# Kernel tuning notes

Hardware: AMD Instinct MI355X
Metric: run time of the kernel (lower is better)

The kernel has to match this reference:

```python
import jax, jax.numpy as jnp
import numpy as np

EPS = 1e-5
N_ENT, N_REL, DIM = 100000, 500, 128
B, K = 2048, 128

def _norm(x):
    # stable L2 norm over last dim, keepdims
    return jnp.sqrt(jnp.sum(x * x, axis=-1, keepdims=True) + 1e-15)

def norm_within_one(x):
    # project onto the open unit ball (Poincare ball, c=1)
    n = _norm(x)
    maxn = 1.0 - EPS
    return jnp.where(n > maxn, x * (maxn / n), x)

def p_log_map(x):
    # log map at the origin: artanh(||x||) * x / ||x||
    n = jnp.clip(_norm(x), EPS, 1.0 - EPS)
    return jnp.arctanh(n) * x / n

def p_exp_map(v):
    # exp map at the origin: tanh(||v||) * v / ||v||
    n = jnp.clip(_norm(v), EPS, None)
    return jnp.tanh(n) * v / n

def p_sum(x, y):
    # Mobius addition (c=1)
    xy = jnp.sum(x * y, axis=-1, keepdims=True)
    x2 = jnp.sum(x * x, axis=-1, keepdims=True)
    y2 = jnp.sum(y * y, axis=-1, keepdims=True)
    num = (1.0 + 2.0 * xy + y2) * x + (1.0 - x2) * y
    den = 1.0 + 2.0 * xy + x2 * y2
    return num / jnp.clip(den, EPS, None)

def calculate_dist(x, y):
    # Poincare distance: arccosh(1 + 2||x-y||^2 / ((1-||x||^2)(1-||y||^2)))
    x2 = jnp.sum(x * x, axis=-1)
    y2 = jnp.sum(y * y, axis=-1)
    d2 = jnp.sum((x - y) ** 2, axis=-1)
    arg = 1.0 + 2.0 * d2 / jnp.clip((1.0 - x2) * (1.0 - y2), EPS, None)
    return jnp.arccosh(jnp.clip(arg, 1.0 + 1e-7, None))

def setup_inputs() -> dict:
    key = jax.random.key(0)
    k1, k2, k3, k4, k5, k6 = jax.random.split(key, 6)
    Eh = 0.001 * jax.random.normal(k1, (N_ENT, DIM), dtype=jnp.float32)
    rvh = 0.001 * jax.random.normal(k2, (N_REL, DIM), dtype=jnp.float32)
    W = jax.random.uniform(k3, (N_REL, DIM), dtype=jnp.float32, minval=-1.0, maxval=1.0)
    bias0 = jnp.zeros((N_ENT,), dtype=jnp.float32)
    bias1 = jnp.zeros((N_ENT,), dtype=jnp.float32)
    head_idx = jax.random.randint(k4, (B, K), 0, N_ENT)
    rel_idx = jax.random.randint(k5, (B, K), 0, N_REL)
    tail_idx = jax.random.randint(k6, (B, K), 0, N_ENT)
    return {"Eh": Eh, "rvh": rvh, "W": W, "bias0": bias0, "bias1": bias1,
            "head_idx": head_idx, "rel_idx": rel_idx, "tail_idx": tail_idx}

def reference(Eh, rvh, W, bias0, bias1, head_idx, rel_idx, tail_idx):
    # gather + project to ball
    h = norm_within_one(Eh[head_idx])          # [B,K,D]
    t = norm_within_one(Eh[tail_idx])          # [B,K,D]
    r = norm_within_one(rvh[rel_idx])          # [B,K,D]
    w = W[rel_idx]                             # [B,K,D]
    # head transform: log map -> diagonal relation scaling -> exp map
    head = norm_within_one(p_exp_map(p_log_map(h) * w))
    # tail transform: Mobius translation by relation vector
    tail = norm_within_one(p_sum(t, r))
    dist = calculate_dist(head, tail)          # [B,K]
    local_bias = bias0[head_idx] + bias1[tail_idx]
    return -dist + local_bias
```

## Files before the change

### kernel.cpp

```cpp
#include <hip/hip_runtime.h>
#include <math.h>


#define EPSF 1e-5f
#define MAXN (1.0f - 1e-5f)

__device__ __forceinline__ float dot4(const float4 a, const float4 b) {
    return a.x * b.x + a.y * b.y + a.z * b.z + a.w * b.w;
}

__global__ __launch_bounds__(256, 4) void poincare_score_kernel(
    const float* __restrict__ Eh, const float* __restrict__ rvh,
    const float* __restrict__ W, const float* __restrict__ bias0,
    const float* __restrict__ bias1, const int* __restrict__ head_idx,
    const int* __restrict__ rel_idx, const int* __restrict__ tail_idx,
    float* __restrict__ out, int total)
{
    const int tid   = threadIdx.x;
    const int lane4 = tid & 3;
    const int e     = blockIdx.x * 64 + (tid >> 2);
    if (e >= total) return;

    const int hi = head_idx[e];
    const int ri = rel_idx[e];
    const int ti = tail_idx[e];

    const float4* __restrict__ Eh4  = reinterpret_cast<const float4*>(Eh);
    const float4* __restrict__ rvh4 = reinterpret_cast<const float4*>(rvh);
    const float4* __restrict__ W4   = reinterpret_cast<const float4*>(W);

    const float4* __restrict__ hrow = Eh4  + (size_t)hi * 32 + lane4;
    const float4* __restrict__ trow = Eh4  + (size_t)ti * 32 + lane4;
    const float4* __restrict__ rrow = rvh4 + (size_t)ri * 32 + lane4;
    const float4* __restrict__ wrow = W4   + (size_t)ri * 32 + lane4;

    float4 h[8], t[8];
#pragma unroll
    for (int j = 0; j < 8; ++j) h[j] = hrow[j * 4];
#pragma unroll
    for (int j = 0; j < 8; ++j) t[j] = trow[j * 4];

    float H2 = 0.f, T2 = 0.f, R2 = 0.f, TR = 0.f;
    float HW2 = 0.f, HWT = 0.f, HWR = 0.f;
#pragma unroll
    for (int j = 0; j < 8; ++j) {
        float4 r = rrow[j * 4];
        float4 w = wrow[j * 4];
        float4 hw;
        hw.x = h[j].x * w.x; hw.y = h[j].y * w.y;
        hw.z = h[j].z * w.z; hw.w = h[j].w * w.w;
        H2  += dot4(h[j], h[j]);
        T2  += dot4(t[j], t[j]);
        R2  += dot4(r, r);
        TR  += dot4(t[j], r);
        HW2 += dot4(hw, hw);
        HWT += dot4(hw, t[j]);
        HWR += dot4(hw, r);
    }

#pragma unroll
    for (int m = 1; m <= 2; m <<= 1) {
        H2  += __shfl_xor(H2,  m);
        T2  += __shfl_xor(T2,  m);
        R2  += __shfl_xor(R2,  m);
        TR  += __shfl_xor(TR,  m);
        HW2 += __shfl_xor(HW2, m);
        HWT += __shfl_xor(HWT, m);
        HWR += __shfl_xor(HWR, m);
    }

    float nh = sqrtf(H2 + 1e-15f);
    float sh = (nh > MAXN) ? (MAXN / nh) : 1.0f;
    float h2 = H2 * sh * sh;

    float nt = sqrtf(T2 + 1e-15f);
    float st = (nt > MAXN) ? (MAXN / nt) : 1.0f;
    float t2 = T2 * st * st;

    float nr = sqrtf(R2 + 1e-15f);
    float sr = (nr > MAXN) ? (MAXN / nr) : 1.0f;
    float r2 = R2 * sr * sr;

    float xy = TR * st * sr;

    float nl = sqrtf(h2 + 1e-15f);
    nl = fminf(fmaxf(nl, EPSF), MAXN);
    float lf = 0.5f * logf((1.0f + nl) / (1.0f - nl)) / nl;
    float a0 = lf * sh;
    float v2 = a0 * a0 * HW2;

    float nv = fmaxf(sqrtf(v2 + 1e-15f), EPSF);
    float ef = tanhf(nv) / nv;
    float b0 = ef * a0;
    float hd2 = b0 * b0 * HW2;

    float nhd = sqrtf(hd2 + 1e-15f);
    float shd = (nhd > MAXN) ? (MAXN / nhd) : 1.0f;
    float b = b0 * shd;
    hd2 = b * b * HW2;

    float ct  = 1.0f + 2.0f * xy + r2;
    float cr  = 1.0f - t2;
    float den = fmaxf(1.0f + 2.0f * xy + t2 * r2, EPSF);
    float id  = 1.0f / den;
    float p = id * ct * st;
    float q = id * cr * sr;
    float tl2 = p * p * T2 + 2.0f * p * q * TR + q * q * R2;

    float ntl = sqrtf(tl2 + 1e-15f);
    float stl = (ntl > MAXN) ? (MAXN / ntl) : 1.0f;
    p *= stl; q *= stl;
    tl2 = tl2 * stl * stl;

    float hdtl = b * (p * HWT + q * HWR);
    float d2   = hd2 + tl2 - 2.0f * hdtl;
    float dn   = fmaxf((1.0f - hd2) * (1.0f - tl2), EPSF);
    float arg  = fmaxf(1.0f + 2.0f * d2 / dn, 1.0f + 1e-7f);
    float dist = acoshf(arg);

    if (lane4 == 0) {
        out[e] = bias0[hi] + bias1[ti] - dist;
    }
}

extern "C" void kernel_launch(void* const* d_in, const int* in_sizes, int n_in,
                              void* d_out, int out_size, void* d_ws, size_t ws_size,
                              hipStream_t stream) {
    const float* Eh       = (const float*)d_in[0];
    const float* rvh      = (const float*)d_in[1];
    const float* W        = (const float*)d_in[2];
    const float* bias0    = (const float*)d_in[3];
    const float* bias1    = (const float*)d_in[4];
    const int*   head_idx = (const int*)d_in[5];
    const int*   rel_idx  = (const int*)d_in[6];
    const int*   tail_idx = (const int*)d_in[7];
    float* out = (float*)d_out;

    const int total  = in_sizes[5];
    const int blocks = (total + 63) / 64;

    poincare_score_kernel<<<blocks, 256, 0, stream>>>(
        Eh, rvh, W, bias0, bias1, head_idx, rel_idx, tail_idx, out, total);
}
```

Before: 48.63 us.

## Convert entity table to bf16 in workspace and gather bf16 rows

```diff
diff --git a/kernel.cpp b/kernel.cpp
--- a/kernel.cpp
+++ b/kernel.cpp
@@ -9,7 +9,153 @@
     return a.x * b.x + a.y * b.y + a.z * b.z + a.w * b.w;
 }
 
-__global__ __launch_bounds__(256, 4) void poincare_score_kernel(
+__device__ __forceinline__ unsigned bfpack(unsigned lo, unsigned hi) {
+    unsigned bl = (lo + 0x7FFFu + ((lo >> 16) & 1u)) >> 16;
+    unsigned bh = (hi + 0x7FFFu + ((hi >> 16) & 1u)) & 0xFFFF0000u;
+    return (bl & 0xFFFFu) | bh;
+}
+
+__global__ __launch_bounds__(256) void cvt_bf16_kernel(
+    const uint4* __restrict__ src, uint4* __restrict__ dst, int ngroups)
+{
+    int i = blockIdx.x * 256 + threadIdx.x;
+    if (i >= ngroups) return;
+    uint4 a = src[2 * i];
+    uint4 b = src[2 * i + 1];
+    uint4 o;
+    o.x = bfpack(a.x, a.y);
+    o.y = bfpack(a.z, a.w);
+    o.z = bfpack(b.x, b.y);
+    o.w = bfpack(b.z, b.w);
+    dst[i] = o;
+}
+
+__device__ __forceinline__ float bflo(unsigned u) { return __uint_as_float(u << 16); }
+__device__ __forceinline__ float bfhi(unsigned u) { return __uint_as_float(u & 0xFFFF0000u); }
+
+__global__ __launch_bounds__(256) void poincare_score_bf16_kernel(
+    const uint4* __restrict__ Ehb, const float* __restrict__ rvh,
+    const float* __restrict__ W, const float* __restrict__ bias0,
+    const float* __restrict__ bias1, const int* __restrict__ head_idx,
+    const int* __restrict__ rel_idx, const int* __restrict__ tail_idx,
+    float* __restrict__ out, int total)
+{
+    const int tid   = threadIdx.x;
+    const int lane4 = tid & 3;
+    const int e     = blockIdx.x * 64 + (tid >> 2);
+    if (e >= total) return;
+
+    const int hi = head_idx[e];
+    const int ri = rel_idx[e];
+    const int ti = tail_idx[e];
+
+    const float4* __restrict__ rvh4 = reinterpret_cast<const float4*>(rvh);
+    const float4* __restrict__ W4   = reinterpret_cast<const float4*>(W);
+
+    const uint4* __restrict__ hrow = Ehb + (size_t)hi * 16 + lane4;
+    const uint4* __restrict__ trow = Ehb + (size_t)ti * 16 + lane4;
+    const float4* __restrict__ rrow = rvh4 + (size_t)ri * 32 + lane4 * 2;
+    const float4* __restrict__ wrow = W4   + (size_t)ri * 32 + lane4 * 2;
+
+    float H2 = 0.f, T2 = 0.f, R2 = 0.f, TR = 0.f;
+    float HW2 = 0.f, HWT = 0.f, HWR = 0.f;
+
+#pragma unroll
+    for (int j = 0; j < 4; ++j) {
+        uint4 hq = hrow[j * 4];
+        uint4 tq = trow[j * 4];
+        float4 r0 = rrow[j * 8],     r1 = rrow[j * 8 + 1];
+        float4 w0 = wrow[j * 8],     w1 = wrow[j * 8 + 1];
+
+        float h0 = bflo(hq.x), h1 = bfhi(hq.x), h2_ = bflo(hq.y), h3 = bfhi(hq.y);
+        float h4 = bflo(hq.z), h5 = bfhi(hq.z), h6 = bflo(hq.w), h7 = bfhi(hq.w);
+        float t0 = bflo(tq.x), t1 = bfhi(tq.x), t2_ = bflo(tq.y), t3 = bfhi(tq.y);
+        float t4 = bflo(tq.z), t5 = bfhi(tq.z), t6 = bflo(tq.w), t7 = bfhi(tq.w);
+
+        float4 ha = make_float4(h0, h1, h2_, h3);
+        float4 hb = make_float4(h4, h5, h6, h7);
+        float4 ta = make_float4(t0, t1, t2_, t3);
+        float4 tb = make_float4(t4, t5, t6, t7);
+
+        float4 hwa, hwb;
+        hwa.x = ha.x * w0.x; hwa.y = ha.y * w0.y; hwa.z = ha.z * w0.z; hwa.w = ha.w * w0.w;
+        hwb.x = hb.x * w1.x; hwb.y = hb.y * w1.y; hwb.z = hb.z * w1.z; hwb.w = hb.w * w1.w;
+
+        H2  += dot4(ha, ha)  + dot4(hb, hb);
+        T2  += dot4(ta, ta)  + dot4(tb, tb);
+        R2  += dot4(r0, r0)  + dot4(r1, r1);
+        TR  += dot4(ta, r0)  + dot4(tb, r1);
+        HW2 += dot4(hwa, hwa) + dot4(hwb, hwb);
+        HWT += dot4(hwa, ta) + dot4(hwb, tb);
+        HWR += dot4(hwa, r0) + dot4(hwb, r1);
+    }
+
+#pragma unroll
+    for (int m = 1; m <= 2; m <<= 1) {
+        H2  += __shfl_xor(H2,  m);
+        T2  += __shfl_xor(T2,  m);
+        R2  += __shfl_xor(R2,  m);
+        TR  += __shfl_xor(TR,  m);
+        HW2 += __shfl_xor(HW2, m);
+        HWT += __shfl_xor(HWT, m);
+        HWR += __shfl_xor(HWR, m);
+    }
+
+    float nh = sqrtf(H2 + 1e-15f);
+    float sh = (nh > MAXN) ? (MAXN / nh) : 1.0f;
+    float h2 = H2 * sh * sh;
+
+    float nt = sqrtf(T2 + 1e-15f);
+    float st = (nt > MAXN) ? (MAXN / nt) : 1.0f;
+    float t2 = T2 * st * st;
+
+    float nr = sqrtf(R2 + 1e-15f);
+    float sr = (nr > MAXN) ? (MAXN / nr) : 1.0f;
+    float r2 = R2 * sr * sr;
+
+    float xy = TR * st * sr;
+
+    float nl = sqrtf(h2 + 1e-15f);
+    nl = fminf(fmaxf(nl, EPSF), MAXN);
+    float lf = 0.5f * logf((1.0f + nl) / (1.0f - nl)) / nl;
+    float a0 = lf * sh;
+    float v2 = a0 * a0 * HW2;
+
+    float nv = fmaxf(sqrtf(v2 + 1e-15f), EPSF);
+    float ef = tanhf(nv) / nv;
+    float b0 = ef * a0;
+    float hd2 = b0 * b0 * HW2;
+
+    float nhd = sqrtf(hd2 + 1e-15f);
+    float shd = (nhd > MAXN) ? (MAXN / nhd) : 1.0f;
+    float b = b0 * shd;
+    hd2 = b * b * HW2;
+
+    float ct  = 1.0f + 2.0f * xy + r2;
+    float cr  = 1.0f - t2;
+    float den = fmaxf(1.0f + 2.0f * xy + t2 * r2, EPSF);
+    float id  = 1.0f / den;
+    float p = id * ct * st;
+    float q = id * cr * sr;
+    float tl2 = p * p * T2 + 2.0f * p * q * TR + q * q * R2;
+
+    float ntl = sqrtf(tl2 + 1e-15f);
+    float stl = (ntl > MAXN) ? (MAXN / ntl) : 1.0f;
+    p *= stl; q *= stl;
+    tl2 = tl2 * stl * stl;
+
+    float hdtl = b * (p * HWT + q * HWR);
+    float d2   = hd2 + tl2 - 2.0f * hdtl;
+    float dn   = fmaxf((1.0f - hd2) * (1.0f - tl2), EPSF);
+    float arg  = fmaxf(1.0f + 2.0f * d2 / dn, 1.0f + 1e-7f);
+    float dist = acoshf(arg);
+
+    if (lane4 == 0) {
+        out[e] = bias0[hi] + bias1[ti] - dist;
+    }
+}
+
+__global__ __launch_bounds__(256) void poincare_score_f32_kernel(
     const float* __restrict__ Eh, const float* __restrict__ rvh,
     const float* __restrict__ W, const float* __restrict__ bias0,
     const float* __restrict__ bias1, const int* __restrict__ head_idx,
@@ -34,30 +180,24 @@
     const float4* __restrict__ rrow = rvh4 + (size_t)ri * 32 + lane4;
     const float4* __restrict__ wrow = W4   + (size_t)ri * 32 + lane4;
 
-    float4 h[8], t[8];
-#pragma unroll
-    for (int j = 0; j < 8; ++j) h[j] = hrow[j * 4];
-#pragma unroll
-    for (int j = 0; j < 8; ++j) t[j] = trow[j * 4];
-
     float H2 = 0.f, T2 = 0.f, R2 = 0.f, TR = 0.f;
     float HW2 = 0.f, HWT = 0.f, HWR = 0.f;
 #pragma unroll
     for (int j = 0; j < 8; ++j) {
+        float4 h = hrow[j * 4];
+        float4 t = trow[j * 4];
         float4 r = rrow[j * 4];
         float4 w = wrow[j * 4];
         float4 hw;
-        hw.x = h[j].x * w.x; hw.y = h[j].y * w.y;
-        hw.z = h[j].z * w.z; hw.w = h[j].w * w.w;
-        H2  += dot4(h[j], h[j]);
-        T2  += dot4(t[j], t[j]);
+        hw.x = h.x * w.x; hw.y = h.y * w.y; hw.z = h.z * w.z; hw.w = h.w * w.w;
+        H2  += dot4(h, h);
+        T2  += dot4(t, t);
         R2  += dot4(r, r);
-        TR  += dot4(t[j], r);
+        TR  += dot4(t, r);
         HW2 += dot4(hw, hw);
-        HWT += dot4(hw, t[j]);
+        HWT += dot4(hw, t);
         HWR += dot4(hw, r);
     }
-
 #pragma unroll
     for (int m = 1; m <= 2; m <<= 1) {
         H2  += __shfl_xor(H2,  m);
@@ -72,15 +212,12 @@
     float nh = sqrtf(H2 + 1e-15f);
     float sh = (nh > MAXN) ? (MAXN / nh) : 1.0f;
     float h2 = H2 * sh * sh;
-
     float nt = sqrtf(T2 + 1e-15f);
     float st = (nt > MAXN) ? (MAXN / nt) : 1.0f;
     float t2 = T2 * st * st;
-
     float nr = sqrtf(R2 + 1e-15f);
     float sr = (nr > MAXN) ? (MAXN / nr) : 1.0f;
     float r2 = R2 * sr * sr;
-
     float xy = TR * st * sr;
 
     float nl = sqrtf(h2 + 1e-15f);
@@ -88,12 +225,10 @@
     float lf = 0.5f * logf((1.0f + nl) / (1.0f - nl)) / nl;
     float a0 = lf * sh;
     float v2 = a0 * a0 * HW2;
-
     float nv = fmaxf(sqrtf(v2 + 1e-15f), EPSF);
     float ef = tanhf(nv) / nv;
     float b0 = ef * a0;
     float hd2 = b0 * b0 * HW2;
-
     float nhd = sqrtf(hd2 + 1e-15f);
     float shd = (nhd > MAXN) ? (MAXN / nhd) : 1.0f;
     float b = b0 * shd;
@@ -106,7 +241,6 @@
     float p = id * ct * st;
     float q = id * cr * sr;
     float tl2 = p * p * T2 + 2.0f * p * q * TR + q * q * R2;
-
     float ntl = sqrtf(tl2 + 1e-15f);
     float stl = (ntl > MAXN) ? (MAXN / ntl) : 1.0f;
     p *= stl; q *= stl;
@@ -139,6 +273,19 @@
     const int total  = in_sizes[5];
     const int blocks = (total + 63) / 64;
 
-    poincare_score_kernel<<<blocks, 256, 0, stream>>>(
-        Eh, rvh, W, bias0, bias1, head_idx, rel_idx, tail_idx, out, total);
-}
+    const int n_eh = in_sizes[0];
+    const size_t need = (size_t)n_eh * 2;
+
+    if (ws_size >= need && (n_eh & 7) == 0) {
+        const int ngroups = n_eh / 8;
+        const int cblocks = (ngroups + 255) / 256;
+        cvt_bf16_kernel<<<cblocks, 256, 0, stream>>>(
+            (const uint4*)Eh, (uint4*)d_ws, ngroups);
+        poincare_score_bf16_kernel<<<blocks, 256, 0, stream>>>(
+            (const uint4*)d_ws, rvh, W, bias0, bias1,
+            head_idx, rel_idx, tail_idx, out, total);
+    } else {
+        poincare_score_f32_kernel<<<blocks, 256, 0, stream>>>(
+            Eh, rvh, W, bias0, bias1, head_idx, rel_idx, tail_idx, out, total);
+    }
+}
```

Measured after the change: 56.99 us. +17.2%, slower.
